# Kernel optimization log

Hardware: AMD Instinct MI355X
Metric: run time of the kernel (lower is better)

The kernel has to match this reference:

```python
import jax, jax.numpy as jnp
import numpy as np

H, W = 48, 96          # fmap_size
HEADS, DH = 4, 128     # BoTNet attention defaults
EPS = 1e-5


def rel_to_abs(x):
    # x: (B, L, 2L-1) relative logits -> (B, L, L) absolute logits
    b, l, _ = x.shape
    x = jnp.pad(x, ((0, 0), (0, 0), (0, 1)))          # (B, L, 2L)
    x = x.reshape(b, l * 2 * l)
    x = jnp.pad(x, ((0, 0), (0, l - 1)))               # (B, (L+1)(2L-1))
    x = x.reshape(b, l + 1, 2 * l - 1)
    return x[:, :l, l - 1:]


def relative_logits_1d(q, rel_k):
    # q: (b, n, X, Y, d), rel_k: (2Y-1, d) -> (b, n, X, X, Y, Y)
    b, n, X, Y, d = q.shape
    logits = jnp.einsum('bnxyd,rd->bnxyr', q, rel_k)
    logits = rel_to_abs(logits.reshape(b * n * X, Y, 2 * Y - 1)).reshape(b, n, X, Y, Y)
    return jnp.broadcast_to(logits[:, :, :, None], (b, n, X, X, Y, Y))


def rel_pos_bias(q, rel_h, rel_w):
    # q: (b, n, H*W, d) already scaled -> (b, n, H*W, H*W)
    b, n, _, d = q.shape
    q2 = q.reshape(b, n, H, W, d)
    lw = relative_logits_1d(q2, rel_w)                     # (b,n,hq,hk,wq,wk)
    lw = lw.transpose(0, 1, 2, 4, 3, 5).reshape(b, n, H * W, H * W)
    qt = q2.transpose(0, 1, 3, 2, 4)                       # (b,n,W,H,d)
    lh = relative_logits_1d(qt, rel_h)                     # (b,n,wq,wk,hq,hk)
    lh = lh.transpose(0, 1, 4, 2, 5, 3).reshape(b, n, H * W, H * W)
    return lw + lh


def bn(x, g, b_, m, v):
    # inference-mode BatchNorm2d over channel dim of (B,C,H,W)
    inv = g * jax.lax.rsqrt(v + EPS)
    return (x - m[:, None, None]) * inv[:, None, None] + b_[:, None, None]


def reference(x, w_in, bn1_g, bn1_b, bn1_m, bn1_v, w_qkv, rel_h, rel_w,
              w_out, bn2_g, bn2_b, bn2_m, bn2_v, w_head, b_head):
    b = x.shape[0]
    # Self_Attn (BoTNet BottleBlock): 1x1 conv down-proj + BN + ReLU
    h1 = jax.nn.relu(bn(jnp.einsum('bcxy,oc->boxy', x, w_in), bn1_g, bn1_b, bn1_m, bn1_v))
    # qkv via 1x1 conv (no bias), chunk into q,k,v blocks along channels
    qkv = jnp.einsum('bcxy,oc->boxy', h1, w_qkv).reshape(b, 3, HEADS, DH, H * W)
    q = qkv[:, 0].transpose(0, 1, 3, 2) * (DH ** -0.5)     # (b, heads, HW, dh)
    k = qkv[:, 1].transpose(0, 1, 3, 2)
    v = qkv[:, 2].transpose(0, 1, 3, 2)
    sim = jnp.einsum('bhid,bhjd->bhij', q, k) + rel_pos_bias(q, rel_h, rel_w)
    attn = jax.nn.softmax(sim, axis=-1)
    out = jnp.einsum('bhij,bhjd->bhid', attn, v)           # (b, heads, HW, dh)
    out = out.transpose(0, 1, 3, 2).reshape(b, HEADS * DH, H, W)
    # 1x1 conv up-proj + BN, residual (dim==dim_out so shortcut=identity), ReLU
    h2 = bn(jnp.einsum('bcxy,oc->boxy', out, w_out), bn2_g, bn2_b, bn2_m, bn2_v)
    fm = jax.nn.relu(h2 + x)
    # Head's final 1x1 conv projection to out_planes
    return jnp.einsum('bcxy,oc->boxy', fm, w_head) + b_head[None, :, None, None]


def setup_inputs() -> dict:
    key = jax.random.key(0)
    ks = jax.random.split(key, 8)
    f = lambda k, s, sc: jax.random.normal(k, s, jnp.float32) * sc
    C_IN, C_MID, C_ATT, C_OUT = 256, 256, 64, 19
    return {
        'x': jax.random.normal(ks[0], (1, C_IN, H, W), jnp.float32),
        'w_in': f(ks[1], (C_ATT, C_IN), 0.05),
        'bn1_g': jnp.ones(C_ATT, jnp.float32), 'bn1_b': jnp.zeros(C_ATT, jnp.float32),
        'bn1_m': jnp.zeros(C_ATT, jnp.float32), 'bn1_v': jnp.ones(C_ATT, jnp.float32),
        'w_qkv': f(ks[2], (3 * HEADS * DH, C_ATT), 0.05),
        'rel_h': f(ks[3], (2 * H - 1, DH), 0.09),
        'rel_w': f(ks[4], (2 * W - 1, DH), 0.09),
        'w_out': f(ks[5], (C_MID, HEADS * DH), 0.02),
        'bn2_g': jnp.ones(C_MID, jnp.float32), 'bn2_b': jnp.zeros(C_MID, jnp.float32),
        'bn2_m': jnp.zeros(C_MID, jnp.float32), 'bn2_v': jnp.ones(C_MID, jnp.float32),
        'w_head': f(ks[6], (C_OUT, C_MID), 0.05),
        'b_head': jnp.zeros(C_OUT, jnp.float32),
    }
```

## Files before the change

kernel.cpp:

```cpp
#include <hip/hip_runtime.h>


typedef __attribute__((ext_vector_type(4))) float f32x4;
typedef __attribute__((ext_vector_type(8))) short s16x8;
typedef __attribute__((ext_vector_type(4))) unsigned short u16x4;

#define HW_N 4608
#define EPS 1e-5f
#define QSCALE 0.08838834764831845f

__device__ __forceinline__ unsigned short f2bf(float f) {
  unsigned u = __builtin_bit_cast(unsigned, f);
  u += 0x7fffu + ((u >> 16) & 1u);
  return (unsigned short)(u >> 16);
}
__device__ __forceinline__ float bf2f(unsigned short s) {
  return __builtin_bit_cast(float, ((unsigned)s) << 16);
}

__global__ __launch_bounds__(256) void conv1_kernel(
    const float* __restrict__ x, const float* __restrict__ w,
    const float* __restrict__ gg, const float* __restrict__ bb,
    const float* __restrict__ mm, const float* __restrict__ vv,
    float* __restrict__ h1)
{
  __shared__ __align__(16) unsigned char smA[16384];
  __shared__ __align__(16) unsigned char smB[16384];
  const int tid = (int)threadIdx.x;
  const int tx = tid & 15, ty = tid >> 4;
  const int p0 = (int)blockIdx.x * 64;
  float acc[4][4] = {};
  for (int ch = 0; ch < 4; ++ch) {
    __syncthreads();
#pragma unroll
    for (int pass = 0; pass < 4; ++pass) {
      int c4 = tid + pass * 256;
      int oc = c4 >> 4, cc4 = c4 & 15;
      f32x4 a = *(const f32x4*)(w + oc * 256 + ch * 64 + cc4 * 4);
#pragma unroll
      for (int k = 0; k < 4; ++k) {
        int cc = cc4 * 4 + k;
        *(float*)(smA + cc * 256 + ((oc * 4) ^ ((cc & 7) << 4))) = a[k];
      }
      int cc = c4 >> 4, pp4 = c4 & 15;
      f32x4 b = *(const f32x4*)(x + (ch * 64 + cc) * HW_N + p0 + pp4 * 4);
      *(f32x4*)(smB + cc * 256 + ((pp4 * 16) ^ ((cc & 7) << 4))) = b;
    }
    __syncthreads();
#pragma unroll 8
    for (int cc = 0; cc < 64; ++cc) {
      f32x4 av = *(const f32x4*)(smA + cc * 256 + ((ty * 16) ^ ((cc & 7) << 4)));
      f32x4 bv = *(const f32x4*)(smB + cc * 256 + ((tx * 16) ^ ((cc & 7) << 4)));
#pragma unroll
      for (int i = 0; i < 4; ++i)
#pragma unroll
        for (int j = 0; j < 4; ++j) acc[i][j] = fmaf(av[i], bv[j], acc[i][j]);
    }
  }
#pragma unroll
  for (int i = 0; i < 4; ++i) {
    int oc = ty * 4 + i;
    float inv = gg[oc] * rsqrtf(vv[oc] + EPS);
    float bia = bb[oc] - mm[oc] * inv;
    f32x4 o;
#pragma unroll
    for (int j = 0; j < 4; ++j) o[j] = fmaxf(acc[i][j] * inv + bia, 0.f);
    *(f32x4*)(h1 + oc * HW_N + p0 + tx * 4) = o;
  }
}

__global__ __launch_bounds__(256) void convqkv_kernel(
    const float* __restrict__ h1, const float* __restrict__ w,
    unsigned short* __restrict__ qb, unsigned short* __restrict__ kb,
    unsigned short* __restrict__ vb)
{
  __shared__ __align__(16) unsigned char smA[16384];
  __shared__ __align__(16) unsigned char smB[16384];
  const int tid = (int)threadIdx.x;
  const int tx = tid & 15, ty = tid >> 4;
  const int p0 = (int)blockIdx.x * 64;
  const int o0 = (int)blockIdx.y * 64;
  float acc[4][4] = {};
#pragma unroll
  for (int pass = 0; pass < 4; ++pass) {
    int c4 = tid + pass * 256;
    int oc = c4 >> 4, cc4 = c4 & 15;
    f32x4 a = *(const f32x4*)(w + (o0 + oc) * 64 + cc4 * 4);
#pragma unroll
    for (int k = 0; k < 4; ++k) {
      int cc = cc4 * 4 + k;
      *(float*)(smA + cc * 256 + ((oc * 4) ^ ((cc & 7) << 4))) = a[k];
    }
    int cc = c4 >> 4, pp4 = c4 & 15;
    f32x4 b = *(const f32x4*)(h1 + cc * HW_N + p0 + pp4 * 4);
    *(f32x4*)(smB + cc * 256 + ((pp4 * 16) ^ ((cc & 7) << 4))) = b;
  }
  __syncthreads();
#pragma unroll 8
  for (int cc = 0; cc < 64; ++cc) {
    f32x4 av = *(const f32x4*)(smA + cc * 256 + ((tx * 16) ^ ((cc & 7) << 4)));
    f32x4 bv = *(const f32x4*)(smB + cc * 256 + ((ty * 16) ^ ((cc & 7) << 4)));
#pragma unroll
    for (int i = 0; i < 4; ++i)
#pragma unroll
      for (int j = 0; j < 4; ++j) acc[i][j] = fmaf(av[i], bv[j], acc[i][j]);
  }
  const int chunk = o0 >> 9, head = (o0 >> 7) & 3, dbase = o0 & 127;
  if (chunk == 0) {
#pragma unroll
    for (int j = 0; j < 4; ++j) {
      unsigned short pk[4];
#pragma unroll
      for (int i = 0; i < 4; ++i) pk[i] = f2bf(acc[i][j] * QSCALE);
      *(unsigned long long*)(qb + (head * HW_N + p0 + ty * 4 + j) * 128 + dbase + tx * 4) =
          *(unsigned long long*)pk;
    }
  } else if (chunk == 1) {
#pragma unroll
    for (int j = 0; j < 4; ++j) {
      unsigned short pk[4];
#pragma unroll
      for (int i = 0; i < 4; ++i) pk[i] = f2bf(acc[i][j]);
      *(unsigned long long*)(kb + (head * HW_N + p0 + ty * 4 + j) * 128 + dbase + tx * 4) =
          *(unsigned long long*)pk;
    }
  } else {
#pragma unroll
    for (int i = 0; i < 4; ++i) {
      unsigned short pk[4];
#pragma unroll
      for (int j = 0; j < 4; ++j) pk[j] = f2bf(acc[i][j]);
      *(unsigned long long*)(vb + (head * 128 + dbase + tx * 4 + i) * HW_N + p0 + ty * 4) =
          *(unsigned long long*)pk;
    }
  }
}

__global__ __launch_bounds__(256) void relpre_mfma(
    const unsigned short* __restrict__ qb, const float* __restrict__ rel,
    float* __restrict__ outp, int mode)
{
  __shared__ __align__(16) unsigned char sm[36864];
  const int bx = (int)blockIdx.x, h = (int)blockIdx.y;
  const int tid = (int)threadIdx.x;
  const int wv = tid >> 6, g = (tid >> 4) & 3, c = tid & 15;
  const int NA = mode ? 96 : 48;
  const int NB = mode ? 48 : 96;
  const int TC = NB >> 4;
  const int roff = mode ? (47 - bx) : (95 - bx);
  unsigned char* const smQ = sm;
  unsigned char* const smR = sm + NA * 256;

  for (int ch = tid; ch < (NA + NB) * 16; ch += 256) {
    if (ch < NA * 16) {
      int i = ch >> 4, d8 = ch & 15;
      int p = mode ? (bx * 96 + i) : (i * 96 + bx);
      s16x8 v = *(const s16x8*)(qb + ((size_t)h * HW_N + p) * 128 + d8 * 8);
      *(s16x8*)(smQ + i * 256 + ((d8 * 16) ^ ((i & 7) << 4))) = v;
    } else {
      int c2 = ch - NA * 16;
      int j = c2 >> 4, d8 = c2 & 15;
      const float* rp = rel + (roff + j) * 128 + d8 * 8;
      f32x4 r0 = *(const f32x4*)(rp);
      f32x4 r1 = *(const f32x4*)(rp + 4);
      s16x8 pk;
#pragma unroll
      for (int e = 0; e < 4; ++e) {
        pk[e] = (short)f2bf(r0[e]);
        pk[4 + e] = (short)f2bf(r1[e]);
      }
      *(s16x8*)(smR + j * 256 + ((d8 * 16) ^ ((j & 7) << 4))) = pk;
    }
  }
  __syncthreads();

  const int swzc = (c & 7) << 4;
  for (int tile = wv; tile < 18; tile += 4) {
    const int tr = tile / TC, tc = tile % TC;
    f32x4 acc = {};
#pragma unroll
    for (int kk = 0; kk < 4; ++kk) {
      const int koff = (kk * 64 + g * 16) ^ swzc;
      s16x8 a = *(const s16x8*)(smQ + (tr * 16 + c) * 256 + koff);
      s16x8 b = *(const s16x8*)(smR + (tc * 16 + c) * 256 + koff);
      acc = __builtin_amdgcn_mfma_f32_16x16x32_bf16(a, b, acc, 0, 0, 0);
    }
#pragma unroll
    for (int j = 0; j < 4; ++j) {
      int i = tr * 16 + g * 4 + j;
      int n = tc * 16 + c;
      if (mode == 0)
        outp[((size_t)h * HW_N + i * 96 + bx) * 96 + n] = acc[j];
      else
        outp[((size_t)h * HW_N + bx * 96 + i) * 48 + n] = acc[j];
    }
  }
}

__global__ __launch_bounds__(256, 2) void attn_kernel(
    const unsigned short* __restrict__ qb,
    const unsigned short* __restrict__ kbuf,
    const unsigned short* __restrict__ vbuf,
    const float* __restrict__ RW,
    const float* __restrict__ RH,
    unsigned short* __restrict__ Opart,
    float* __restrict__ mlbuf)
{
  __shared__ __align__(16) unsigned char sm[36864];
  unsigned char* const smK = sm;
  unsigned char* const smV = sm + 12288;
  unsigned char* const smP = sm + 28672;

  const int tid = (int)threadIdx.x;
  const int wv = tid >> 6;
  const int g = (tid >> 4) & 3;
  const int c = tid & 15;
  const int swzc = (c & 7) << 4;
  const int pswz_c = ((c >> 2) << 5) | ((c & 1) << 4);

  int lin = (int)blockIdx.x + 72 * ((int)blockIdx.y + 4 * (int)blockIdx.z);
  const int grp = lin & 15, mem = lin >> 4;
  const int h = grp & 3, kh = grp >> 2, qt = mem;

  const int qbase = qt * 64 + wv * 16;
  const int woff = wv * 2048;

  {
    s16x8 z = {};
    *(s16x8*)(smP + tid * 16) = z;
    *(s16x8*)(smP + 4096 + tid * 16) = z;
    int d = tid >> 1, k6 = 6 + (tid & 1);
    *(s16x8*)(smV + d * 128 + ((k6 * 16) ^ ((d & 7) << 4))) = z;
  }

  s16x8 aq[4];
  {
    const unsigned short* qrow = qb + ((size_t)h * HW_N + qbase + c) * 128 + g * 8;
#pragma unroll
    for (int kk = 0; kk < 4; ++kk) aq[kk] = *(const s16x8*)(qrow + kk * 32);
  }

  float bw0[3][4], bw1[3][4];
#pragma unroll
  for (int r = 0; r < 4; ++r) {
    const float* rwrow = RW + ((size_t)h * HW_N + qbase + g * 4 + r) * 96 + c;
#pragma unroll
    for (int kb = 0; kb < 3; ++kb) {
      bw0[kb][r] = rwrow[kb * 16];
      bw1[kb][r] = rwrow[48 + kb * 16];
    }
  }
  float rh_pre[4];
#pragma unroll
  for (int r = 0; r < 4; ++r)
    rh_pre[r] = (c < 12)
        ? RH[((size_t)h * HW_N + qbase + g * 4 + r) * 48 + kh * 12 + c] : 0.f;

  f32x4 o[8];
#pragma unroll
  for (int cb = 0; cb < 8; ++cb) o[cb] = {};
  float mrun[4], lrun[4];
#pragma unroll
  for (int r = 0; r < 4; ++r) { mrun[r] = -1e30f; lrun[r] = 0.f; }

  const unsigned short* kbase = kbuf + ((size_t)h * HW_N + kh * 1152) * 128;
  const unsigned short* vbase = vbuf + (size_t)h * 128 * HW_N + kh * 1152;

  const int kkey = tid >> 4, kd8 = tid & 15;
  const int swzk = (kkey & 7) << 4;
  const int vd0 = tid / 6, vk0 = tid % 6;
  const int vd1 = (tid + 256) / 6, vk1 = (tid + 256) % 6;
  const int vd2 = (tid + 512) / 6, vk2 = (tid + 512) % 6;

  s16x8 sK0, sK1, sK2, sV0, sV1, sV2;
  {
    const unsigned short* kp = kbase + kkey * 128 + kd8 * 8;
    sK0 = *(const s16x8*)(kp);
    sK1 = *(const s16x8*)(kp + 16 * 128);
    sK2 = *(const s16x8*)(kp + 32 * 128);
    sV0 = *(const s16x8*)(vbase + vd0 * HW_N + vk0 * 8);
    sV1 = *(const s16x8*)(vbase + vd1 * HW_N + vk1 * 8);
    sV2 = *(const s16x8*)(vbase + vd2 * HW_N + vk2 * 8);
  }

  for (int t = 0; t < 24; ++t) {
    __syncthreads();
    *(s16x8*)(smK + kkey * 256 + ((kd8 * 16) ^ swzk)) = sK0;
    *(s16x8*)(smK + (kkey + 16) * 256 + ((kd8 * 16) ^ swzk)) = sK1;
    *(s16x8*)(smK + (kkey + 32) * 256 + ((kd8 * 16) ^ swzk)) = sK2;
    *(s16x8*)(smV + vd0 * 128 + ((vk0 * 16) ^ ((vd0 & 7) << 4))) = sV0;
    *(s16x8*)(smV + vd1 * 128 + ((vk1 * 16) ^ ((vd1 & 7) << 4))) = sV1;
    *(s16x8*)(smV + vd2 * 128 + ((vk2 * 16) ^ ((vd2 & 7) << 4))) = sV2;
    if (t < 23) {
      int j0n = (t + 1) * 48;
      const unsigned short* kp = kbase + (j0n + kkey) * 128 + kd8 * 8;
      sK0 = *(const s16x8*)(kp);
      sK1 = *(const s16x8*)(kp + 16 * 128);
      sK2 = *(const s16x8*)(kp + 32 * 128);
      sV0 = *(const s16x8*)(vbase + vd0 * HW_N + j0n + vk0 * 8);
      sV1 = *(const s16x8*)(vbase + vd1 * HW_N + j0n + vk1 * 8);
      sV2 = *(const s16x8*)(vbase + vd2 * HW_N + j0n + vk2 * 8);
    }
    float rh_[4];
    {
      const int hkl = t >> 1;
#pragma unroll
      for (int r = 0; r < 4; ++r) rh_[r] = __shfl(rh_pre[r], hkl, 16);
    }
    __syncthreads();

    f32x4 s0 = {}, s1 = {}, s2 = {};
#pragma unroll
    for (int kk = 0; kk < 4; ++kk) {
      const int inr = kk * 64 + g * 16;
      s16x8 b0 = *(const s16x8*)(smK + c * 256 + (inr ^ swzc));
      s16x8 b1 = *(const s16x8*)(smK + (16 + c) * 256 + (inr ^ swzc));
      s16x8 b2 = *(const s16x8*)(smK + (32 + c) * 256 + (inr ^ swzc));
      s0 = __builtin_amdgcn_mfma_f32_16x16x32_bf16(aq[kk], b0, s0, 0, 0, 0);
      s1 = __builtin_amdgcn_mfma_f32_16x16x32_bf16(aq[kk], b1, s1, 0, 0, 0);
      s2 = __builtin_amdgcn_mfma_f32_16x16x32_bf16(aq[kk], b2, s2, 0, 0, 0);
    }

    const bool par = (t & 1) != 0;
    float x0[4], x1[4], x2[4], tm3[4];
    int need = 0;
#pragma unroll
    for (int r = 0; r < 4; ++r) {
      x0[r] = s0[r] + (par ? bw1[0][r] : bw0[0][r]) + rh_[r];
      x1[r] = s1[r] + (par ? bw1[1][r] : bw0[1][r]) + rh_[r];
      x2[r] = s2[r] + (par ? bw1[2][r] : bw0[2][r]) + rh_[r];
      tm3[r] = fmaxf(fmaxf(x0[r], x1[r]), x2[r]);
      need |= (tm3[r] > mrun[r] + 8.f);
    }
    if (__any(need)) {
#pragma unroll
      for (int r = 0; r < 4; ++r) {
        float tg = tm3[r];
        tg = fmaxf(tg, __shfl_xor(tg, 1, 16));
        tg = fmaxf(tg, __shfl_xor(tg, 2, 16));
        tg = fmaxf(tg, __shfl_xor(tg, 4, 16));
        tg = fmaxf(tg, __shfl_xor(tg, 8, 16));
        float mn = fmaxf(mrun[r], tg);
        float fac = __expf(mrun[r] - mn);
        mrun[r] = mn;
        lrun[r] *= fac;
#pragma unroll
        for (int cb = 0; cb < 8; ++cb) o[cb][r] *= fac;
      }
    }
#pragma unroll
    for (int r = 0; r < 4; ++r) {
      float p0 = __expf(x0[r] - mrun[r]);
      float p1 = __expf(x1[r] - mrun[r]);
      float p2 = __expf(x2[r] - mrun[r]);
      lrun[r] += p0 + p1 + p2;
      const int q_ = g * 4 + r;
      unsigned char* prow = smP + woff + q_ * 128;
      const int swzq = ((q_ >> 2) << 5) | ((q_ & 1) << 4);
      *(unsigned short*)(prow + ((c * 2) ^ swzq)) = f2bf(p0);
      *(unsigned short*)(prow + ((32 + c * 2) ^ swzq)) = f2bf(p1);
      *(unsigned short*)(prow + ((64 + c * 2) ^ swzq)) = f2bf(p2);
    }

    s16x8 pa0 = *(const s16x8*)(smP + woff + c * 128 + ((g * 16) ^ pswz_c));
    s16x8 pa1 = *(const s16x8*)(smP + woff + c * 128 + ((64 + g * 16) ^ pswz_c));
#pragma unroll
    for (int cb = 0; cb < 8; ++cb) {
      const unsigned char* vrow = smV + (cb * 16 + c) * 128;
      s16x8 v0 = *(const s16x8*)(vrow + ((g * 16) ^ swzc));
      s16x8 v1 = *(const s16x8*)(vrow + ((64 + g * 16) ^ swzc));
      o[cb] = __builtin_amdgcn_mfma_f32_16x16x32_bf16(pa0, v0, o[cb], 0, 0, 0);
      o[cb] = __builtin_amdgcn_mfma_f32_16x16x32_bf16(pa1, v1, o[cb], 0, 0, 0);
    }
  }

#pragma unroll
  for (int r = 0; r < 4; ++r) {
    lrun[r] += __shfl_xor(lrun[r], 1, 16);
    lrun[r] += __shfl_xor(lrun[r], 2, 16);
    lrun[r] += __shfl_xor(lrun[r], 4, 16);
    lrun[r] += __shfl_xor(lrun[r], 8, 16);
  }

  const int pb = (kh * 4 + h) * HW_N;
#pragma unroll
  for (int r = 0; r < 4; ++r) {
    const int p = qbase + g * 4 + r;
    unsigned short* orow = Opart + ((size_t)pb + p) * 128 + c;
#pragma unroll
    for (int cb = 0; cb < 8; ++cb) orow[cb * 16] = f2bf(o[cb][r]);
    if (c == 0) {
      mlbuf[((size_t)pb + p) * 2 + 0] = mrun[r];
      mlbuf[((size_t)pb + p) * 2 + 1] = lrun[r];
    }
  }
}

__global__ __launch_bounds__(256) void merge_kernel(
    const unsigned short* __restrict__ Opart, const float* __restrict__ mlbuf,
    float* __restrict__ oatt)
{
  int idx = (int)blockIdx.x * 256 + (int)threadIdx.x;
  int d4 = idx & 31;
  int rest = idx >> 5;
  int p = rest % HW_N;
  int h = rest / HW_N;
  float m[4], l[4];
#pragma unroll
  for (int s = 0; s < 4; ++s) {
    int ip = (s * 4 + h) * HW_N + p;
    m[s] = mlbuf[(size_t)ip * 2];
    l[s] = mlbuf[(size_t)ip * 2 + 1];
  }
  float M = fmaxf(fmaxf(m[0], m[1]), fmaxf(m[2], m[3]));
  float a[4], den = 0.f;
#pragma unroll
  for (int s = 0; s < 4; ++s) { a[s] = __expf(m[s] - M); den += a[s] * l[s]; }
  float rd = 1.f / den;
  f32x4 acc = {};
#pragma unroll
  for (int s = 0; s < 4; ++s) {
    int ip = (s * 4 + h) * HW_N + p;
    u16x4 ov = *(const u16x4*)(Opart + (size_t)ip * 128 + d4 * 4);
#pragma unroll
    for (int j = 0; j < 4; ++j) acc[j] = fmaf(a[s], bf2f(ov[j]), acc[j]);
  }
  f32x4 res;
#pragma unroll
  for (int j = 0; j < 4; ++j) res[j] = acc[j] * rd;
  *(f32x4*)(oatt + (size_t)p * 512 + h * 128 + d4 * 4) = res;
}

__global__ __launch_bounds__(256) void convout_kernel(
    const float* __restrict__ oatt, const float* __restrict__ w,
    const float* __restrict__ gg, const float* __restrict__ bb,
    const float* __restrict__ mm, const float* __restrict__ vv,
    const float* __restrict__ x, float* __restrict__ fm)
{
  __shared__ __align__(16) unsigned char smA[16384];
  __shared__ __align__(16) unsigned char smB[16384];
  const int tid = (int)threadIdx.x;
  const int tx = tid & 15, ty = tid >> 4;
  const int p0 = (int)blockIdx.x * 64;
  const int o0 = (int)blockIdx.y * 64;
  float acc[4][4] = {};
  for (int ch = 0; ch < 8; ++ch) {
    __syncthreads();
#pragma unroll
    for (int pass = 0; pass < 4; ++pass) {
      int c4 = tid + pass * 256;
      int oc = c4 >> 4, cc4 = c4 & 15;
      f32x4 a = *(const f32x4*)(w + (o0 + oc) * 512 + ch * 64 + cc4 * 4);
#pragma unroll
      for (int k = 0; k < 4; ++k) {
        int cc = cc4 * 4 + k;
        *(float*)(smA + cc * 256 + ((oc * 4) ^ ((cc & 7) << 4))) = a[k];
      }
      int pl = c4 >> 4, cc4b = c4 & 15;
      f32x4 b = *(const f32x4*)(oatt + (size_t)(p0 + pl) * 512 + ch * 64 + cc4b * 4);
#pragma unroll
      for (int k = 0; k < 4; ++k) {
        int cc = cc4b * 4 + k;
        *(float*)(smB + cc * 256 + ((pl * 4) ^ ((cc & 7) << 4))) = b[k];
      }
    }
    __syncthreads();
#pragma unroll 8
    for (int cc = 0; cc < 64; ++cc) {
      f32x4 av = *(const f32x4*)(smA + cc * 256 + ((ty * 16) ^ ((cc & 7) << 4)));
      f32x4 bv = *(const f32x4*)(smB + cc * 256 + ((tx * 16) ^ ((cc & 7) << 4)));
#pragma unroll
      for (int i = 0; i < 4; ++i)
#pragma unroll
        for (int j = 0; j < 4; ++j) acc[i][j] = fmaf(av[i], bv[j], acc[i][j]);
    }
  }
#pragma unroll
  for (int i = 0; i < 4; ++i) {
    int oc = o0 + ty * 4 + i;
    float inv = gg[oc] * rsqrtf(vv[oc] + EPS);
    float bia = bb[oc] - mm[oc] * inv;
    f32x4 xr = *(const f32x4*)(x + (size_t)oc * HW_N + p0 + tx * 4);
    f32x4 o;
#pragma unroll
    for (int j = 0; j < 4; ++j) o[j] = fmaxf(acc[i][j] * inv + bia + xr[j], 0.f);
    *(f32x4*)(fm + (size_t)oc * HW_N + p0 + tx * 4) = o;
  }
}

__global__ __launch_bounds__(256) void convhead_kernel(
    const float* __restrict__ fm, const float* __restrict__ w,
    const float* __restrict__ bh, float* __restrict__ outp)
{
  __shared__ __align__(16) unsigned char smA[16384];
  __shared__ __align__(16) unsigned char smB[16384];
  const int tid = (int)threadIdx.x;
  const int tx = tid & 15, ty = tid >> 4;
  const int p0 = (int)blockIdx.x * 64;
  float acc[4][4] = {};
  for (int ch = 0; ch < 4; ++ch) {
    __syncthreads();
#pragma unroll
    for (int pass = 0; pass < 4; ++pass) {
      int c4 = tid + pass * 256;
      int oc = c4 >> 4, cc4 = c4 & 15;
      f32x4 a = {};
      if (oc < 19) a = *(const f32x4*)(w + oc * 256 + ch * 64 + cc4 * 4);
#pragma unroll
      for (int k = 0; k < 4; ++k) {
        int cc = cc4 * 4 + k;
        *(float*)(smA + cc * 256 + ((oc * 4) ^ ((cc & 7) << 4))) = a[k];
      }
      int cc = c4 >> 4, pp4 = c4 & 15;
      f32x4 b = *(const f32x4*)(fm + (ch * 64 + cc) * HW_N + p0 + pp4 * 4);
      *(f32x4*)(smB + cc * 256 + ((pp4 * 16) ^ ((cc & 7) << 4))) = b;
    }
    __syncthreads();
#pragma unroll 8
    for (int cc = 0; cc < 64; ++cc) {
      f32x4 av = *(const f32x4*)(smA + cc * 256 + ((ty * 16) ^ ((cc & 7) << 4)));
      f32x4 bv = *(const f32x4*)(smB + cc * 256 + ((tx * 16) ^ ((cc & 7) << 4)));
#pragma unroll
      for (int i = 0; i < 4; ++i)
#pragma unroll
        for (int j = 0; j < 4; ++j) acc[i][j] = fmaf(av[i], bv[j], acc[i][j]);
    }
  }
#pragma unroll
  for (int i = 0; i < 4; ++i) {
    int oc = ty * 4 + i;
    if (oc < 19) {
      f32x4 o;
#pragma unroll
      for (int j = 0; j < 4; ++j) o[j] = acc[i][j] + bh[oc];
      *(f32x4*)(outp + oc * HW_N + p0 + tx * 4) = o;
    }
  }
}

extern "C" void kernel_launch(void* const* d_in, const int* in_sizes, int n_in,
                              void* d_out, int out_size, void* d_ws, size_t ws_size,
                              hipStream_t stream)
{
  const float* x     = (const float*)d_in[0];
  const float* w_in  = (const float*)d_in[1];
  const float* bn1_g = (const float*)d_in[2];
  const float* bn1_b = (const float*)d_in[3];
  const float* bn1_m = (const float*)d_in[4];
  const float* bn1_v = (const float*)d_in[5];
  const float* w_qkv = (const float*)d_in[6];
  const float* rel_h = (const float*)d_in[7];
  const float* rel_w = (const float*)d_in[8];
  const float* w_out = (const float*)d_in[9];
  const float* bn2_g = (const float*)d_in[10];
  const float* bn2_b = (const float*)d_in[11];
  const float* bn2_m = (const float*)d_in[12];
  const float* bn2_v = (const float*)d_in[13];
  const float* w_hd  = (const float*)d_in[14];
  const float* b_hd  = (const float*)d_in[15];

  char* ws = (char*)d_ws;
  float*          h1    = (float*)(ws + 0);
  float*          mlb   = (float*)(ws + 0);
  unsigned short* qb    = (unsigned short*)(ws + 1179648);
  unsigned short* kb    = (unsigned short*)(ws + 5898240);
  unsigned short* vb    = (unsigned short*)(ws + 10616832);
  float*          RW    = (float*)(ws + 15335424);
  float*          RH    = (float*)(ws + 22413312);
  unsigned short* Opart = (unsigned short*)(ws + 25952256);
  float*          oatt  = (float*)(ws + 45121536);
  float*          fm    = (float*)(ws + 54558720);

  conv1_kernel<<<72, 256, 0, stream>>>(x, w_in, bn1_g, bn1_b, bn1_m, bn1_v, h1);
  convqkv_kernel<<<dim3(72, 24), 256, 0, stream>>>(h1, w_qkv, qb, kb, vb);
  relpre_mfma<<<dim3(96, 4), 256, 0, stream>>>(qb, rel_w, RW, 0);
  relpre_mfma<<<dim3(48, 4), 256, 0, stream>>>(qb, rel_h, RH, 1);
  attn_kernel<<<dim3(72, 4, 4), 256, 0, stream>>>(qb, kb, vb, RW, RH, Opart, mlb);
  merge_kernel<<<2304, 256, 0, stream>>>(Opart, mlb, oatt);
  convout_kernel<<<dim3(72, 4), 256, 0, stream>>>(oatt, w_out, bn2_g, bn2_b, bn2_m,
                                                  bn2_v, x, fm);
  convhead_kernel<<<72, 256, 0, stream>>>(fm, w_hd, b_hd, (float*)d_out);
}
```

Before: 307.2 us.

## Split attention into six key chunks, merge relpre launches, and port output convs to MFMA

Splits the attention key range into 6 chunks instead of 4 (1152 blocks instead of 1152? now 72x24 grid), so more blocks run in parallel with shorter loops. The merge kernel combines 6 partials and writes bf16. The two relpre launches become one. convout and convhead move from scalar FP32 FMA to bf16 MFMA with global_load_lds staging, using bf16 intermediates. s_setprio is added around the MFMA sections. This lowers precision of the intermediates and reuses the RW/RH workspace region for oatt/fm.

```diff
diff --git a/kernel.cpp b/kernel.cpp
--- a/kernel.cpp
+++ b/kernel.cpp
@@ -16,6 +16,9 @@
 }
 __device__ __forceinline__ float bf2f(unsigned short s) {
   return __builtin_bit_cast(float, ((unsigned)s) << 16);
+}
+__device__ __forceinline__ void gload_lds16(const void* g, void* l) {
+  __builtin_amdgcn_global_load_lds(g, l, 16, 0, 0);
 }
 
 __global__ __launch_bounds__(256) void conv1_kernel(
@@ -137,17 +140,23 @@
 }
 
 __global__ __launch_bounds__(256) void relpre_mfma(
-    const unsigned short* __restrict__ qb, const float* __restrict__ rel,
-    float* __restrict__ outp, int mode)
+    const unsigned short* __restrict__ qb,
+    const float* __restrict__ rel_h, const float* __restrict__ rel_w,
+    float* __restrict__ RW, float* __restrict__ RH)
 {
   __shared__ __align__(16) unsigned char sm[36864];
-  const int bx = (int)blockIdx.x, h = (int)blockIdx.y;
+  int bxr = (int)blockIdx.x;
+  const int mode = bxr >= 96;
+  const int bx = mode ? bxr - 96 : bxr;
+  const int h = (int)blockIdx.y;
   const int tid = (int)threadIdx.x;
   const int wv = tid >> 6, g = (tid >> 4) & 3, c = tid & 15;
   const int NA = mode ? 96 : 48;
   const int NB = mode ? 48 : 96;
   const int TC = NB >> 4;
   const int roff = mode ? (47 - bx) : (95 - bx);
+  const float* rel = mode ? rel_h : rel_w;
+  float* outp = mode ? RH : RW;
   unsigned char* const smQ = sm;
   unsigned char* const smR = sm + NA * 256;
 
@@ -218,9 +227,9 @@
   const int swzc = (c & 7) << 4;
   const int pswz_c = ((c >> 2) << 5) | ((c & 1) << 4);
 
-  int lin = (int)blockIdx.x + 72 * ((int)blockIdx.y + 4 * (int)blockIdx.z);
-  const int grp = lin & 15, mem = lin >> 4;
-  const int h = grp & 3, kh = grp >> 2, qt = mem;
+  const int lin = (int)blockIdx.x + 72 * (int)blockIdx.y;
+  const int grp = lin % 24, qt = lin / 24;
+  const int h = grp & 3, kh = grp >> 2;
 
   const int qbase = qt * 64 + wv * 16;
   const int woff = wv * 2048;
@@ -253,8 +262,8 @@
   float rh_pre[4];
 #pragma unroll
   for (int r = 0; r < 4; ++r)
-    rh_pre[r] = (c < 12)
-        ? RH[((size_t)h * HW_N + qbase + g * 4 + r) * 48 + kh * 12 + c] : 0.f;
+    rh_pre[r] = (c < 8)
+        ? RH[((size_t)h * HW_N + qbase + g * 4 + r) * 48 + kh * 8 + c] : 0.f;
 
   f32x4 o[8];
 #pragma unroll
@@ -263,8 +272,8 @@
 #pragma unroll
   for (int r = 0; r < 4; ++r) { mrun[r] = -1e30f; lrun[r] = 0.f; }
 
-  const unsigned short* kbase = kbuf + ((size_t)h * HW_N + kh * 1152) * 128;
-  const unsigned short* vbase = vbuf + (size_t)h * 128 * HW_N + kh * 1152;
+  const unsigned short* kbase = kbuf + ((size_t)h * HW_N + kh * 768) * 128;
+  const unsigned short* vbase = vbuf + (size_t)h * 128 * HW_N + kh * 768;
 
   const int kkey = tid >> 4, kd8 = tid & 15;
   const int swzk = (kkey & 7) << 4;
@@ -283,7 +292,7 @@
     sV2 = *(const s16x8*)(vbase + vd2 * HW_N + vk2 * 8);
   }
 
-  for (int t = 0; t < 24; ++t) {
+  for (int t = 0; t < 16; ++t) {
     __syncthreads();
     *(s16x8*)(smK + kkey * 256 + ((kd8 * 16) ^ swzk)) = sK0;
     *(s16x8*)(smK + (kkey + 16) * 256 + ((kd8 * 16) ^ swzk)) = sK1;
@@ -291,7 +300,7 @@
     *(s16x8*)(smV + vd0 * 128 + ((vk0 * 16) ^ ((vd0 & 7) << 4))) = sV0;
     *(s16x8*)(smV + vd1 * 128 + ((vk1 * 16) ^ ((vd1 & 7) << 4))) = sV1;
     *(s16x8*)(smV + vd2 * 128 + ((vk2 * 16) ^ ((vd2 & 7) << 4))) = sV2;
-    if (t < 23) {
+    if (t < 15) {
       int j0n = (t + 1) * 48;
       const unsigned short* kp = kbase + (j0n + kkey) * 128 + kd8 * 8;
       sK0 = *(const s16x8*)(kp);
@@ -310,6 +319,7 @@
     __syncthreads();
 
     f32x4 s0 = {}, s1 = {}, s2 = {};
+    __builtin_amdgcn_s_setprio(1);
 #pragma unroll
     for (int kk = 0; kk < 4; ++kk) {
       const int inr = kk * 64 + g * 16;
@@ -320,6 +330,7 @@
       s1 = __builtin_amdgcn_mfma_f32_16x16x32_bf16(aq[kk], b1, s1, 0, 0, 0);
       s2 = __builtin_amdgcn_mfma_f32_16x16x32_bf16(aq[kk], b2, s2, 0, 0, 0);
     }
+    __builtin_amdgcn_s_setprio(0);
 
     const bool par = (t & 1) != 0;
     float x0[4], x1[4], x2[4], tm3[4];
@@ -364,6 +375,7 @@
 
     s16x8 pa0 = *(const s16x8*)(smP + woff + c * 128 + ((g * 16) ^ pswz_c));
     s16x8 pa1 = *(const s16x8*)(smP + woff + c * 128 + ((64 + g * 16) ^ pswz_c));
+    __builtin_amdgcn_s_setprio(1);
 #pragma unroll
     for (int cb = 0; cb < 8; ++cb) {
       const unsigned char* vrow = smV + (cb * 16 + c) * 128;
@@ -372,6 +384,7 @@
       o[cb] = __builtin_amdgcn_mfma_f32_16x16x32_bf16(pa0, v0, o[cb], 0, 0, 0);
       o[cb] = __builtin_amdgcn_mfma_f32_16x16x32_bf16(pa1, v1, o[cb], 0, 0, 0);
     }
+    __builtin_amdgcn_s_setprio(0);
   }
 
 #pragma unroll
@@ -398,144 +411,186 @@
 
 __global__ __launch_bounds__(256) void merge_kernel(
     const unsigned short* __restrict__ Opart, const float* __restrict__ mlbuf,
-    float* __restrict__ oatt)
+    unsigned short* __restrict__ oatt)
 {
   int idx = (int)blockIdx.x * 256 + (int)threadIdx.x;
   int d4 = idx & 31;
   int rest = idx >> 5;
   int p = rest % HW_N;
   int h = rest / HW_N;
-  float m[4], l[4];
-#pragma unroll
-  for (int s = 0; s < 4; ++s) {
+  float m[6], lv[6];
+#pragma unroll
+  for (int s = 0; s < 6; ++s) {
     int ip = (s * 4 + h) * HW_N + p;
     m[s] = mlbuf[(size_t)ip * 2];
-    l[s] = mlbuf[(size_t)ip * 2 + 1];
-  }
-  float M = fmaxf(fmaxf(m[0], m[1]), fmaxf(m[2], m[3]));
-  float a[4], den = 0.f;
-#pragma unroll
-  for (int s = 0; s < 4; ++s) { a[s] = __expf(m[s] - M); den += a[s] * l[s]; }
+    lv[s] = mlbuf[(size_t)ip * 2 + 1];
+  }
+  float M = m[0];
+#pragma unroll
+  for (int s = 1; s < 6; ++s) M = fmaxf(M, m[s]);
+  float a[6], den = 0.f;
+#pragma unroll
+  for (int s = 0; s < 6; ++s) { a[s] = __expf(m[s] - M); den += a[s] * lv[s]; }
   float rd = 1.f / den;
   f32x4 acc = {};
 #pragma unroll
-  for (int s = 0; s < 4; ++s) {
+  for (int s = 0; s < 6; ++s) {
     int ip = (s * 4 + h) * HW_N + p;
     u16x4 ov = *(const u16x4*)(Opart + (size_t)ip * 128 + d4 * 4);
 #pragma unroll
     for (int j = 0; j < 4; ++j) acc[j] = fmaf(a[s], bf2f(ov[j]), acc[j]);
   }
-  f32x4 res;
-#pragma unroll
-  for (int j = 0; j < 4; ++j) res[j] = acc[j] * rd;
-  *(f32x4*)(oatt + (size_t)p * 512 + h * 128 + d4 * 4) = res;
+  u16x4 res;
+#pragma unroll
+  for (int j = 0; j < 4; ++j) res[j] = f2bf(acc[j] * rd);
+  *(u16x4*)(oatt + (size_t)p * 512 + h * 128 + d4 * 4) = res;
 }
 
 __global__ __launch_bounds__(256) void convout_kernel(
-    const float* __restrict__ oatt, const float* __restrict__ w,
+    const unsigned short* __restrict__ oatt, const float* __restrict__ w,
     const float* __restrict__ gg, const float* __restrict__ bb,
     const float* __restrict__ mm, const float* __restrict__ vv,
-    const float* __restrict__ x, float* __restrict__ fm)
-{
-  __shared__ __align__(16) unsigned char smA[16384];
+    const float* __restrict__ x, unsigned short* __restrict__ fm)
+{
+  __shared__ __align__(16) unsigned char smA[8192];
   __shared__ __align__(16) unsigned char smB[16384];
   const int tid = (int)threadIdx.x;
-  const int tx = tid & 15, ty = tid >> 4;
-  const int p0 = (int)blockIdx.x * 64;
+  const int wv = tid >> 6, g = (tid >> 4) & 3, c = tid & 15;
+  const int p0 = (int)blockIdx.x * 128;
   const int o0 = (int)blockIdx.y * 64;
-  float acc[4][4] = {};
+  const int swzc = (c & 7) << 4;
+  const int aoc = tid >> 2, aq4 = tid & 3;
+  const int brow = tid >> 3, bcol = (tid & 7) * 16;
+  f32x4 acc[8];
+#pragma unroll
+  for (int cb = 0; cb < 8; ++cb) acc[cb] = {};
+
   for (int ch = 0; ch < 8; ++ch) {
     __syncthreads();
 #pragma unroll
-    for (int pass = 0; pass < 4; ++pass) {
-      int c4 = tid + pass * 256;
-      int oc = c4 >> 4, cc4 = c4 & 15;
-      f32x4 a = *(const f32x4*)(w + (o0 + oc) * 512 + ch * 64 + cc4 * 4);
-#pragma unroll
-      for (int k = 0; k < 4; ++k) {
-        int cc = cc4 * 4 + k;
-        *(float*)(smA + cc * 256 + ((oc * 4) ^ ((cc & 7) << 4))) = a[k];
-      }
-      int pl = c4 >> 4, cc4b = c4 & 15;
-      f32x4 b = *(const f32x4*)(oatt + (size_t)(p0 + pl) * 512 + ch * 64 + cc4b * 4);
-#pragma unroll
-      for (int k = 0; k < 4; ++k) {
-        int cc = cc4b * 4 + k;
-        *(float*)(smB + cc * 256 + ((pl * 4) ^ ((cc & 7) << 4))) = b[k];
-      }
-    }
-    __syncthreads();
-#pragma unroll 8
-    for (int cc = 0; cc < 64; ++cc) {
-      f32x4 av = *(const f32x4*)(smA + cc * 256 + ((ty * 16) ^ ((cc & 7) << 4)));
-      f32x4 bv = *(const f32x4*)(smB + cc * 256 + ((tx * 16) ^ ((cc & 7) << 4)));
-#pragma unroll
-      for (int i = 0; i < 4; ++i)
-#pragma unroll
-        for (int j = 0; j < 4; ++j) acc[i][j] = fmaf(av[i], bv[j], acc[i][j]);
-    }
-  }
+    for (int i = 0; i < 4; ++i)
+      gload_lds16((const char*)oatt + (size_t)(p0 + i * 32 + brow) * 1024 + ch * 128 +
+                      (bcol ^ ((brow & 7) << 4)),
+                  smB + i * 4096 + wv * 1024);
+    {
+      const float* wp = w + (size_t)(o0 + aoc) * 512 + ch * 64 + aq4 * 16;
+      f32x4 a0 = *(const f32x4*)(wp);
+      f32x4 a1 = *(const f32x4*)(wp + 4);
+      f32x4 a2 = *(const f32x4*)(wp + 8);
+      f32x4 a3 = *(const f32x4*)(wp + 12);
+      s16x8 w0, w1;
+#pragma unroll
+      for (int e = 0; e < 4; ++e) {
+        w0[e] = (short)f2bf(a0[e]); w0[4 + e] = (short)f2bf(a1[e]);
+        w1[e] = (short)f2bf(a2[e]); w1[4 + e] = (short)f2bf(a3[e]);
+      }
+      *(s16x8*)(smA + aoc * 128 + ((aq4 * 32) ^ ((aoc & 7) << 4))) = w0;
+      *(s16x8*)(smA + aoc * 128 + ((aq4 * 32 + 16) ^ ((aoc & 7) << 4))) = w1;
+    }
+    __syncthreads();
+#pragma unroll
+    for (int kk = 0; kk < 2; ++kk) {
+      s16x8 a = *(const s16x8*)(smA + (wv * 16 + c) * 128 + ((kk * 64 + g * 16) ^ swzc));
+#pragma unroll
+      for (int cb = 0; cb < 8; ++cb) {
+        s16x8 b = *(const s16x8*)(smB + (cb * 16 + c) * 128 + ((kk * 64 + g * 16) ^ swzc));
+        acc[cb] = __builtin_amdgcn_mfma_f32_16x16x32_bf16(a, b, acc[cb], 0, 0, 0);
+      }
+    }
+  }
+
+  __syncthreads();
+  float inv[4], bia[4];
+#pragma unroll
+  for (int r = 0; r < 4; ++r) {
+    int oc = o0 + wv * 16 + g * 4 + r;
+    inv[r] = gg[oc] * rsqrtf(vv[oc] + EPS);
+    bia[r] = bb[oc] - mm[oc] * inv[r];
+  }
+#pragma unroll
+  for (int cb = 0; cb < 8; ++cb)
+#pragma unroll
+    for (int r = 0; r < 4; ++r) {
+      int oc = o0 + wv * 16 + g * 4 + r;
+      int p = p0 + cb * 16 + c;
+      float v = fmaxf(acc[cb][r] * inv[r] + bia[r] + x[(size_t)oc * HW_N + p], 0.f);
+      *(unsigned short*)(smB + (cb * 16 + c) * 128 +
+                         (((wv * 16 + g * 4 + r) * 2) ^ swzc)) = f2bf(v);
+    }
+  __syncthreads();
 #pragma unroll
   for (int i = 0; i < 4; ++i) {
-    int oc = o0 + ty * 4 + i;
-    float inv = gg[oc] * rsqrtf(vv[oc] + EPS);
-    float bia = bb[oc] - mm[oc] * inv;
-    f32x4 xr = *(const f32x4*)(x + (size_t)oc * HW_N + p0 + tx * 4);
-    f32x4 o;
-#pragma unroll
-    for (int j = 0; j < 4; ++j) o[j] = fmaxf(acc[i][j] * inv + bia + xr[j], 0.f);
-    *(f32x4*)(fm + (size_t)oc * HW_N + p0 + tx * 4) = o;
+    int row = i * 32 + brow;
+    s16x8 vd = *(const s16x8*)(smB + row * 128 + (bcol ^ ((row & 7) << 4)));
+    *(s16x8*)((char*)fm + (size_t)(p0 + row) * 512 + o0 * 2 + bcol) = vd;
   }
 }
 
 __global__ __launch_bounds__(256) void convhead_kernel(
-    const float* __restrict__ fm, const float* __restrict__ w,
+    const unsigned short* __restrict__ fm, const float* __restrict__ w,
     const float* __restrict__ bh, float* __restrict__ outp)
 {
-  __shared__ __align__(16) unsigned char smA[16384];
+  __shared__ __align__(16) unsigned char smA[4096];
   __shared__ __align__(16) unsigned char smB[16384];
   const int tid = (int)threadIdx.x;
-  const int tx = tid & 15, ty = tid >> 4;
-  const int p0 = (int)blockIdx.x * 64;
-  float acc[4][4] = {};
+  const int wv = tid >> 6, g = (tid >> 4) & 3, c = tid & 15;
+  const int p0 = (int)blockIdx.x * 128;
+  const int swzc = (c & 7) << 4;
+  const int aoc = tid >> 3, aq8 = tid & 7;
+  const int brow = tid >> 3, bcol = (tid & 7) * 16;
+  f32x4 acc[2][2];
+#pragma unroll
+  for (int u = 0; u < 2; ++u)
+#pragma unroll
+    for (int cbi = 0; cbi < 2; ++cbi) acc[u][cbi] = {};
+
   for (int ch = 0; ch < 4; ++ch) {
     __syncthreads();
 #pragma unroll
-    for (int pass = 0; pass < 4; ++pass) {
-      int c4 = tid + pass * 256;
-      int oc = c4 >> 4, cc4 = c4 & 15;
-      f32x4 a = {};
-      if (oc < 19) a = *(const f32x4*)(w + oc * 256 + ch * 64 + cc4 * 4);
-#pragma unroll
-      for (int k = 0; k < 4; ++k) {
-        int cc = cc4 * 4 + k;
-        *(float*)(smA + cc * 256 + ((oc * 4) ^ ((cc & 7) << 4))) = a[k];
-      }
-      int cc = c4 >> 4, pp4 = c4 & 15;
-      f32x4 b = *(const f32x4*)(fm + (ch * 64 + cc) * HW_N + p0 + pp4 * 4);
-      *(f32x4*)(smB + cc * 256 + ((pp4 * 16) ^ ((cc & 7) << 4))) = b;
-    }
-    __syncthreads();
-#pragma unroll 8
-    for (int cc = 0; cc < 64; ++cc) {
-      f32x4 av = *(const f32x4*)(smA + cc * 256 + ((ty * 16) ^ ((cc & 7) << 4)));
-      f32x4 bv = *(const f32x4*)(smB + cc * 256 + ((tx * 16) ^ ((cc & 7) << 4)));
-#pragma unroll
-      for (int i = 0; i < 4; ++i)
-#pragma unroll
-        for (int j = 0; j < 4; ++j) acc[i][j] = fmaf(av[i], bv[j], acc[i][j]);
-    }
-  }
-#pragma unroll
-  for (int i = 0; i < 4; ++i) {
-    int oc = ty * 4 + i;
-    if (oc < 19) {
-      f32x4 o;
-#pragma unroll
-      for (int j = 0; j < 4; ++j) o[j] = acc[i][j] + bh[oc];
-      *(f32x4*)(outp + oc * HW_N + p0 + tx * 4) = o;
-    }
-  }
+    for (int i = 0; i < 4; ++i)
+      gload_lds16((const char*)fm + (size_t)(p0 + i * 32 + brow) * 512 + ch * 128 +
+                      (bcol ^ ((brow & 7) << 4)),
+                  smB + i * 4096 + wv * 1024);
+    {
+      s16x8 w0 = {};
+      if (aoc < 19) {
+        const float* wp = w + (size_t)aoc * 256 + ch * 64 + aq8 * 8;
+        f32x4 a0 = *(const f32x4*)(wp);
+        f32x4 a1 = *(const f32x4*)(wp + 4);
+#pragma unroll
+        for (int e = 0; e < 4; ++e) {
+          w0[e] = (short)f2bf(a0[e]);
+          w0[4 + e] = (short)f2bf(a1[e]);
+        }
+      }
+      *(s16x8*)(smA + aoc * 128 + ((aq8 * 16) ^ ((aoc & 7) << 4))) = w0;
+    }
+    __syncthreads();
+#pragma unroll
+    for (int kk = 0; kk < 2; ++kk) {
+      s16x8 a0 = *(const s16x8*)(smA + c * 128 + ((kk * 64 + g * 16) ^ swzc));
+      s16x8 a1 = *(const s16x8*)(smA + (16 + c) * 128 + ((kk * 64 + g * 16) ^ swzc));
+#pragma unroll
+      for (int cbi = 0; cbi < 2; ++cbi) {
+        int cb = wv * 2 + cbi;
+        s16x8 b = *(const s16x8*)(smB + (cb * 16 + c) * 128 + ((kk * 64 + g * 16) ^ swzc));
+        acc[0][cbi] = __builtin_amdgcn_mfma_f32_16x16x32_bf16(a0, b, acc[0][cbi], 0, 0, 0);
+        acc[1][cbi] = __builtin_amdgcn_mfma_f32_16x16x32_bf16(a1, b, acc[1][cbi], 0, 0, 0);
+      }
+    }
+  }
+#pragma unroll
+  for (int u = 0; u < 2; ++u)
+#pragma unroll
+    for (int cbi = 0; cbi < 2; ++cbi)
+#pragma unroll
+      for (int r = 0; r < 4; ++r) {
+        int oc = u * 16 + g * 4 + r;
+        if (oc < 19) {
+          int p = p0 + (wv * 2 + cbi) * 16 + c;
+          outp[(size_t)oc * HW_N + p] = acc[u][cbi][r] + bh[oc];
+        }
+      }
 }
 
 extern "C" void kernel_launch(void* const* d_in, const int* in_sizes, int n_in,
@@ -567,17 +622,16 @@
   unsigned short* vb    = (unsigned short*)(ws + 10616832);
   float*          RW    = (float*)(ws + 15335424);
   float*          RH    = (float*)(ws + 22413312);
+  unsigned short* oatt  = (unsigned short*)(ws + 15335424);
+  unsigned short* fm    = (unsigned short*)(ws + 20054016);
   unsigned short* Opart = (unsigned short*)(ws + 25952256);
-  float*          oatt  = (float*)(ws + 45121536);
-  float*          fm    = (float*)(ws + 54558720);
 
   conv1_kernel<<<72, 256, 0, stream>>>(x, w_in, bn1_g, bn1_b, bn1_m, bn1_v, h1);
   convqkv_kernel<<<dim3(72, 24), 256, 0, stream>>>(h1, w_qkv, qb, kb, vb);
-  relpre_mfma<<<dim3(96, 4), 256, 0, stream>>>(qb, rel_w, RW, 0);
-  relpre_mfma<<<dim3(48, 4), 256, 0, stream>>>(qb, rel_h, RH, 1);
-  attn_kernel<<<dim3(72, 4, 4), 256, 0, stream>>>(qb, kb, vb, RW, RH, Opart, mlb);
+  relpre_mfma<<<dim3(144, 4), 256, 0, stream>>>(qb, rel_h, rel_w, RW, RH);
+  attn_kernel<<<dim3(72, 24), 256, 0, stream>>>(qb, kb, vb, RW, RH, Opart, mlb);
   merge_kernel<<<2304, 256, 0, stream>>>(Opart, mlb, oatt);
-  convout_kernel<<<dim3(72, 4), 256, 0, stream>>>(oatt, w_out, bn2_g, bn2_b, bn2_m,
+  convout_kernel<<<dim3(36, 4), 256, 0, stream>>>(oatt, w_out, bn2_g, bn2_b, bn2_m,
                                                   bn2_v, x, fm);
-  convhead_kernel<<<72, 256, 0, stream>>>(fm, w_hd, b_hd, (float*)d_out);
-}
+  convhead_kernel<<<36, 256, 0, stream>>>(fm, w_hd, b_hd, (float*)d_out);
+}
```

Result: faster. 249.2 us (-18.9%).
